# Optimization experiments

Measured on AMD Instinct MI355X. Metric: run time of the kernel, lower is better.

Reference implementation:

```python
import jax, jax.numpy as jnp
import numpy as np


def _conv(x, w, b=None, stride=1, pad=0, dil=1):
    out = jax.lax.conv_general_dilated(
        x, w, (stride, stride), [(pad, pad), (pad, pad)],
        rhs_dilation=(dil, dil),
        dimension_numbers=('NCHW', 'OIHW', 'NCHW'))
    return out if b is None else out + b[None, :, None, None]


def _sobel_base(out_ch, in_ch, k=3):
    # Exactly mirrors SobelConv2d weight construction (4 directional kernels).
    w = np.zeros((out_ch, in_ch, k, k), np.float32)
    m = k // 2
    for idx in range(out_ch):
        if idx % 4 == 0:
            w[idx, :, 0, :] = -1; w[idx, :, 0, m] = -2
            w[idx, :, -1, :] = 1; w[idx, :, -1, m] = 2
        elif idx % 4 == 1:
            w[idx, :, :, 0] = -1; w[idx, :, m, 0] = -2
            w[idx, :, :, -1] = 1; w[idx, :, m, -1] = 2
        elif idx % 4 == 2:
            w[idx, :, 0, 0] = -2
            for i in range(m + 1):
                w[idx, :, m - i, i] = -1
                w[idx, :, k - 1 - i, m + i] = 1
            w[idx, :, -1, -1] = 2
        else:
            w[idx, :, -1, 0] = -2
            for i in range(m + 1):
                w[idx, :, m + i, i] = -1
                w[idx, :, i, m + i] = 1
            w[idx, :, 0, -1] = 2
    return w


def setup_inputs() -> dict:
    key = jax.random.key(0)
    ks = iter(jax.random.split(key, 40))
    def p(shape, s=0.05):
        return jax.random.normal(next(ks), shape, dtype=jnp.float32) * s
    C = 32  # out_ch == sobel_ch
    f32 = jnp.float32
    return dict(
        x=jax.random.normal(next(ks), (8, 1, 256, 256), dtype=f32),
        sobel_base=jnp.asarray(_sobel_base(C, 1)),
        sobel_factor=jnp.ones((C, 1, 1, 1), f32),
        sobel_bias=jnp.zeros((C,), f32),
        f4_w=p((C, C + 1, 3, 3)), f4_b=jnp.zeros((C,), f32),
        ec1_w=p((C, C, 3, 3)), ec1_b=jnp.zeros((C,), f32),
        ec2_w=p((C, C, 3, 3)), ec2_b=jnp.zeros((C,), f32),
        ec3_w=p((C, C, 3, 3)), ec3_b=jnp.zeros((C,), f32),
        gate_w=p((3, 3 * C, 1, 1)), gate_b=jnp.zeros((3,), f32),
        ca1_w=p((C // 16, C, 1, 1)),  # ChannelAttention fc1 (ratio=16), no bias
        ca2_w=p((C, C // 16, 1, 1)),  # fc2, no bias
        sa_w=p((1, 2, 7, 7)),         # SpatialAttention conv, no bias
        p1_w=p((C, C, 1, 1)), p1_b=jnp.zeros((C,), f32),
        f1_w=p((C, C, 3, 3)), f1_b=jnp.zeros((C,), f32),
        p2_w=p((C, 2 * C, 1, 1)), p2_b=jnp.zeros((C,), f32),
        f2_w=p((C, C, 3, 3)), f2_b=jnp.zeros((C,), f32),
        p3_w=p((C, 2 * C, 1, 1)), p3_b=jnp.zeros((C,), f32),
        f3_w=p((C, C, 3, 3)), f3_b=jnp.zeros((C,), f32),
    )


def reference(x, sobel_base, sobel_factor, sobel_bias, f4_w, f4_b,
              ec1_w, ec1_b, ec2_w, ec2_b, ec3_w, ec3_b, gate_w, gate_b,
              ca1_w, ca2_w, sa_w,
              p1_w, p1_b, f1_w, f1_b, p2_w, p2_b, f2_w, f2_b,
              p3_w, p3_b, f3_w, f3_b):
    lrelu = lambda t: jax.nn.leaky_relu(t, 0.01)
    relu = jax.nn.relu
    # Sobel edge extraction (fixed directional kernels scaled by learned factor)
    out0 = _conv(x, sobel_base * sobel_factor, sobel_bias, pad=1)     # [B,32,H,W]
    out1 = jnp.concatenate([x, out0], axis=1)                          # [B,33,H,W]
    out1 = lrelu(_conv(out1, f4_w, f4_b, pad=1))                       # [B,32,H,W]
    # AdaptiveEdgeConnector: multi-dilation convs + softmax gating
    ex = relu(_conv(out1, ec1_w, ec1_b, pad=1))
    ey = relu(_conv(out1, ec2_w, ec2_b, pad=2, dil=2))
    ez = relu(_conv(out1, ec3_w, ec3_b, pad=3, dil=3))
    gates = jax.nn.softmax(_conv(jnp.concatenate([ex, ey, ez], axis=1), gate_w, gate_b), axis=1)
    enh = gates[:, 0:1] * ex + gates[:, 1:2] * ey + gates[:, 2:3] * ez
    # CBAM: channel attention
    avg = jnp.mean(enh, axis=(2, 3), keepdims=True)
    mx = jnp.max(enh, axis=(2, 3), keepdims=True)
    ca = jax.nn.sigmoid(_conv(relu(_conv(avg, ca1_w)), ca2_w)
                        + _conv(relu(_conv(mx, ca1_w)), ca2_w))
    f = ca * enh
    # CBAM: spatial attention
    sa_in = jnp.concatenate([jnp.mean(f, axis=1, keepdims=True),
                             jnp.max(f, axis=1, keepdims=True)], axis=1)
    sa = jax.nn.sigmoid(_conv(sa_in, sa_w, pad=3))
    edge = sa * f
    # Residual merge + cascaded dense conv stages
    out0 = lrelu(out1 + edge)
    t = lrelu(_conv(out0, p1_w, p1_b))
    t = lrelu(_conv(t, f1_w, f1_b, pad=1))
    o1 = jnp.concatenate([out0, t], axis=1)                            # [B,64,H,W]
    t = lrelu(_conv(o1, p2_w, p2_b))
    t = lrelu(_conv(t, f2_w, f2_b, pad=1))
    o2 = jnp.concatenate([out0, t], axis=1)
    t = lrelu(_conv(o2, p3_w, p3_b))
    t = lrelu(_conv(t, f3_w, f3_b, pad=1))
    return jnp.concatenate([out0, t], axis=1)                          # [B,64,H,W]
```

## Files before the change

### kernel.cpp

```cpp
#include <hip/hip_runtime.h>
#include <math.h>

typedef unsigned short u16;
typedef short short8 __attribute__((ext_vector_type(8)));
typedef float f32x4 __attribute__((ext_vector_type(4)));
typedef unsigned short ushort4v __attribute__((ext_vector_type(4)));

#define Hh 256
#define Ww 256
#define Bb 8
#define PW 262
#define PAD 3
#define HPW (Hh * PW)

__device__ __forceinline__ float bf2f(u16 v) {
    unsigned u = ((unsigned)v) << 16;
    union { unsigned u; float f; } c; c.u = u; return c.f;
}
__device__ __forceinline__ u16 f2bf(float f) {
    union { float f; unsigned u; } c; c.f = f;
    unsigned lsb = (c.u >> 16) & 1u;
    c.u += 0x7fffu + lsb;
    return (u16)(c.u >> 16);
}
__device__ __forceinline__ float sigm(float v) { return 1.f / (1.f + expf(-v)); }

template<int ACT, bool F32OUT, bool FUSEP>
__global__ __launch_bounds__(256) void convs_k(
    const u16* __restrict__ in, const u16* __restrict__ apack,
    const float* __restrict__ bias, void* __restrict__ outp,
    const u16* __restrict__ o0buf, const u16* __restrict__ pw,
    const float* __restrict__ pb, u16* __restrict__ pout)
{
    __shared__ u16 rows[3][4352];
    const int tid = threadIdx.x, lane = tid & 63, wv = tid >> 6;
    const int b = blockIdx.x & 7;
    const int rest = blockIdx.x >> 3;
    const int h = rest >> 1, half = rest & 1;
    const int pl = wv * 32 + (lane & 15);
    const int icg = lane >> 4;

    for (int idx = tid; idx < 3 * 536; idx += 256) {
        int rr = idx / 536, q = idx % 536;
        int r = h - 1 + rr;
        short8 v = (short8){0, 0, 0, 0, 0, 0, 0, 0};
        if ((unsigned)r < 256u)
            v = *(const short8*)(in + ((size_t)b * HPW + (size_t)r * PW + PAD + half * 128 - 3) * 32
                                 + (size_t)q * 8);
        *(short8*)(&rows[rr][q * 8]) = v;
    }
    __syncthreads();

    f32x4 acc[2][2];
    #pragma unroll
    for (int mf = 0; mf < 2; ++mf)
        #pragma unroll
        for (int nf = 0; nf < 2; ++nf)
            acc[mf][nf] = (f32x4){0.f, 0.f, 0.f, 0.f};

    #pragma unroll
    for (int tap = 0; tap < 9; ++tap) {
        const int kh = tap / 3 - 1, kw = tap % 3 - 1;
        const int ri = 1 + kh;
        short8 a0 = *(const short8*)(apack + ((size_t)(tap * 2 + 0) * 64 + lane) * 8);
        short8 a1 = *(const short8*)(apack + ((size_t)(tap * 2 + 1) * 64 + lane) * 8);
        #pragma unroll
        for (int nf = 0; nf < 2; ++nf) {
            short8 bf = *(const short8*)(&rows[ri][(pl + nf * 16 + kw + 3) * 32 + icg * 8]);
            acc[0][nf] = __builtin_amdgcn_mfma_f32_16x16x32_bf16(a0, bf, acc[0][nf], 0, 0, 0);
            acc[1][nf] = __builtin_amdgcn_mfma_f32_16x16x32_bf16(a1, bf, acc[1][nf], 0, 0, 0);
        }
    }
    const int nl = half * 128 + pl;
    f32x4 bi[2];
    bi[0] = *(const f32x4*)(bias + icg * 4);
    bi[1] = *(const f32x4*)(bias + 16 + icg * 4);

    if (FUSEP) {
        u16* tile = &rows[0][0];
        __syncthreads();
        #pragma unroll
        for (int mf = 0; mf < 2; ++mf) {
            const int cob = mf * 16 + icg * 4;
            #pragma unroll
            for (int nf = 0; nf < 2; ++nf) {
                ushort4v o;
                #pragma unroll
                for (int i = 0; i < 4; ++i) {
                    float v = acc[mf][nf][i] + bi[mf][i];
                    v = (v > 0.f) ? v : 0.01f * v;
                    o[i] = f2bf(v);
                }
                *(ushort4v*)(tile + (pl + nf * 16) * 32 + cob) = o;
            }
        }
        __syncthreads();
        f32x4 acc2[2][2];
        #pragma unroll
        for (int mf = 0; mf < 2; ++mf)
            #pragma unroll
            for (int nf = 0; nf < 2; ++nf)
                acc2[mf][nf] = (f32x4){0.f, 0.f, 0.f, 0.f};
        #pragma unroll
        for (int s = 0; s < 2; ++s) {
            short8 pa0 = *(const short8*)(pw + (size_t)(s * 2 + 0) * 512 + lane * 8);
            short8 pa1 = *(const short8*)(pw + (size_t)(s * 2 + 1) * 512 + lane * 8);
            #pragma unroll
            for (int nf = 0; nf < 2; ++nf) {
                const int px = pl + nf * 16;
                short8 bf;
                if (s == 0)
                    bf = *(const short8*)(o0buf + ((size_t)b * HPW + (size_t)h * PW + PAD + half * 128 + px) * 32 + icg * 8);
                else
                    bf = *(const short8*)(tile + px * 32 + icg * 8);
                acc2[0][nf] = __builtin_amdgcn_mfma_f32_16x16x32_bf16(pa0, bf, acc2[0][nf], 0, 0, 0);
                acc2[1][nf] = __builtin_amdgcn_mfma_f32_16x16x32_bf16(pa1, bf, acc2[1][nf], 0, 0, 0);
            }
        }
        const size_t orow = ((size_t)b * HPW + (size_t)h * PW + PAD) * 32;
        #pragma unroll
        for (int mf = 0; mf < 2; ++mf) {
            const int cob = mf * 16 + icg * 4;
            f32x4 pbi = *(const f32x4*)(pb + cob);
            #pragma unroll
            for (int nf = 0; nf < 2; ++nf) {
                ushort4v o;
                #pragma unroll
                for (int i = 0; i < 4; ++i) {
                    float v = acc2[mf][nf][i] + pbi[i];
                    v = (v > 0.f) ? v : 0.01f * v;
                    o[i] = f2bf(v);
                }
                *(ushort4v*)(pout + orow + (size_t)(nl + nf * 16) * 32 + cob) = o;
            }
        }
        if (tid < 12) {
            int col3 = tid >> 2, chunk = tid & 3;
            int col = half ? (256 + PAD + col3) : col3;
            u16* pz = pout + ((size_t)b * HPW + (size_t)h * PW + col) * 32 + chunk * 8;
            *(short8*)pz = (short8){0, 0, 0, 0, 0, 0, 0, 0};
        }
    } else if (F32OUT) {
        float* dp = (float*)outp + ((size_t)b * 64 + 32) * 65536 + (size_t)h * 256;
        #pragma unroll
        for (int mf = 0; mf < 2; ++mf) {
            const int cob = mf * 16 + icg * 4;
            #pragma unroll
            for (int nf = 0; nf < 2; ++nf) {
                const int w = nl + nf * 16;
                #pragma unroll
                for (int i = 0; i < 4; ++i) {
                    float v = acc[mf][nf][i] + bi[mf][i];
                    if (ACT == 1) v = fmaxf(v, 0.f);
                    if (ACT == 2) v = (v > 0.f) ? v : 0.01f * v;
                    dp[(size_t)(cob + i) * 65536 + w] = v;
                }
            }
        }
    } else {
        const size_t orow = ((size_t)b * HPW + (size_t)h * PW + PAD) * 32;
        u16* out = (u16*)outp;
        #pragma unroll
        for (int mf = 0; mf < 2; ++mf) {
            const int cob = mf * 16 + icg * 4;
            #pragma unroll
            for (int nf = 0; nf < 2; ++nf) {
                ushort4v o;
                #pragma unroll
                for (int i = 0; i < 4; ++i) {
                    float v = acc[mf][nf][i] + bi[mf][i];
                    if (ACT == 1) v = fmaxf(v, 0.f);
                    if (ACT == 2) v = (v > 0.f) ? v : 0.01f * v;
                    o[i] = f2bf(v);
                }
                *(ushort4v*)(out + orow + (size_t)(nl + nf * 16) * 32 + cob) = o;
            }
        }
    }
}

__global__ __launch_bounds__(256) void ecfuse_k(
    const u16* __restrict__ in, const u16* __restrict__ apack,
    const float* __restrict__ b1, const float* __restrict__ b2,
    const float* __restrict__ b3, const float* __restrict__ gw_,
    const float* __restrict__ gb_, u16* __restrict__ enh)
{
    __shared__ u16 rows[3][4352];
    __shared__ float gw[288];
    __shared__ float gb[3];
    __shared__ float bs[96];
    int tid = threadIdx.x;
    for (int i = tid; i < 288; i += 256) gw[i] = gw_[i];
    if (tid < 3) gb[tid] = gb_[tid];
    if (tid < 32) bs[tid] = b1[tid];
    else if (tid < 64) bs[tid] = b2[tid - 32];
    else if (tid < 96) bs[tid] = b3[tid - 64];

    const int lane = tid & 63, wv = tid >> 6;
    const int b = blockIdx.x & 7;
    const int rest = blockIdx.x >> 3;
    const int h = rest >> 1, half = rest & 1;
    const int pl = wv * 32 + (lane & 15);
    const int icg = lane >> 4;

    f32x4 acc[3][2][2];
    #pragma unroll
    for (int cv = 0; cv < 3; ++cv)
        #pragma unroll
        for (int mf = 0; mf < 2; ++mf)
            #pragma unroll
            for (int nf = 0; nf < 2; ++nf)
                acc[cv][mf][nf] = (f32x4){0.f, 0.f, 0.f, 0.f};

    #pragma unroll
    for (int cv = 0; cv < 3; ++cv) {
        const int dil = cv + 1;
        __syncthreads();
        for (int idx = tid; idx < 3 * 536; idx += 256) {
            int rr = idx / 536, q = idx % 536;
            int r = h + (rr - 1) * dil;
            short8 v = (short8){0, 0, 0, 0, 0, 0, 0, 0};
            if ((unsigned)r < 256u)
                v = *(const short8*)(in + ((size_t)b * HPW + (size_t)r * PW + PAD + half * 128 - 3) * 32
                                     + (size_t)q * 8);
            *(short8*)(&rows[rr][q * 8]) = v;
        }
        __syncthreads();
        const u16* ap = apack + (size_t)(cv * 9 * 2) * 512;
        #pragma unroll
        for (int tap = 0; tap < 9; ++tap) {
            const int kh = tap / 3 - 1, kw = tap % 3 - 1;
            const int ri = 1 + kh;
            short8 a0 = *(const short8*)(ap + (size_t)(tap * 2 + 0) * 512 + lane * 8);
            short8 a1 = *(const short8*)(ap + (size_t)(tap * 2 + 1) * 512 + lane * 8);
            #pragma unroll
            for (int nf = 0; nf < 2; ++nf) {
                short8 bf = *(const short8*)(&rows[ri][(pl + nf * 16 + kw * dil + 3) * 32 + icg * 8]);
                acc[cv][0][nf] = __builtin_amdgcn_mfma_f32_16x16x32_bf16(a0, bf, acc[cv][0][nf], 0, 0, 0);
                acc[cv][1][nf] = __builtin_amdgcn_mfma_f32_16x16x32_bf16(a1, bf, acc[cv][1][nf], 0, 0, 0);
            }
        }
    }
    const int nl = half * 128 + pl;
    const size_t orow = ((size_t)b * HPW + (size_t)h * PW + PAD) * 32;
    #pragma unroll
    for (int nf = 0; nf < 2; ++nf) {
        float e[3][2][4];
        float g0 = 0.f, g1 = 0.f, g2 = 0.f;
        #pragma unroll
        for (int cv = 0; cv < 3; ++cv)
            #pragma unroll
            for (int mf = 0; mf < 2; ++mf) {
                const int cob = mf * 16 + icg * 4;
                #pragma unroll
                for (int i = 0; i < 4; ++i) {
                    float v = fmaxf(acc[cv][mf][nf][i] + bs[cv * 32 + cob + i], 0.f);
                    e[cv][mf][i] = v;
                    const int c = cv * 32 + cob + i;
                    g0 = fmaf(gw[c], v, g0);
                    g1 = fmaf(gw[96 + c], v, g1);
                    g2 = fmaf(gw[192 + c], v, g2);
                }
            }
        g0 += __shfl_xor(g0, 16); g0 += __shfl_xor(g0, 32);
        g1 += __shfl_xor(g1, 16); g1 += __shfl_xor(g1, 32);
        g2 += __shfl_xor(g2, 16); g2 += __shfl_xor(g2, 32);
        g0 += gb[0]; g1 += gb[1]; g2 += gb[2];
        float m = fmaxf(g0, fmaxf(g1, g2));
        float e0 = expf(g0 - m), e1 = expf(g1 - m), e2 = expf(g2 - m);
        float inv = 1.f / (e0 + e1 + e2);
        e0 *= inv; e1 *= inv; e2 *= inv;
        #pragma unroll
        for (int mf = 0; mf < 2; ++mf) {
            const int cob = mf * 16 + icg * 4;
            ushort4v o;
            #pragma unroll
            for (int i = 0; i < 4; ++i)
                o[i] = f2bf(e0 * e[0][mf][i] + e1 * e[1][mf][i] + e2 * e[2][mf][i]);
            *(ushort4v*)(enh + orow + (size_t)(nl + nf * 16) * 32 + cob) = o;
        }
    }
}

__global__ void prepack_k(
    const float* __restrict__ f4w, const float* __restrict__ e1w,
    const float* __restrict__ e2w, const float* __restrict__ e3w,
    const float* __restrict__ f1w, const float* __restrict__ f2w,
    const float* __restrict__ f3w, const float* __restrict__ p1w,
    const float* __restrict__ p2w, const float* __restrict__ p3w,
    u16* __restrict__ apack)
{
    int gid = blockIdx.x * 256 + threadIdx.x;
    if (gid >= 77 * 1024) return;
    const int offs[11] = {0, 18, 27, 36, 45, 54, 63, 72, 73, 75, 77};
    int step = gid >> 10, r = gid & 1023;
    int layer = 0;
    while (step >= offs[layer + 1]) layer++;
    int s = step - offs[layer];
    int mf = r >> 9, l = (r >> 3) & 63, j = r & 7;
    int co = mf * 16 + (l & 15);
    int ICB = (layer == 0 || layer == 8 || layer == 9) ? 2 : 1;
    int tap = s / ICB, icb = s % ICB;
    int icl = icb * 32 + (l >> 4) * 8 + j;
    float v = 0.f;
    if (layer == 0)      { if (icl < 33) v = f4w[(co * 33 + icl) * 9 + tap]; }
    else if (layer == 1) v = e1w[(co * 32 + icl) * 9 + tap];
    else if (layer == 2) v = e2w[(co * 32 + icl) * 9 + tap];
    else if (layer == 3) v = e3w[(co * 32 + icl) * 9 + tap];
    else if (layer == 4) v = f1w[(co * 32 + icl) * 9 + tap];
    else if (layer == 5) v = f2w[(co * 32 + icl) * 9 + tap];
    else if (layer == 6) v = f3w[(co * 32 + icl) * 9 + tap];
    else if (layer == 7) v = p1w[co * 32 + icl];
    else if (layer == 8) v = p2w[co * 64 + icl];
    else                 v = p3w[co * 64 + icl];
    apack[gid] = f2bf(v);
}

__global__ __launch_bounds__(256) void prep5_k(
    const float* __restrict__ f4w, const float* __restrict__ f4b,
    const float* __restrict__ sbase, const float* __restrict__ sfac,
    const float* __restrict__ sbias,
    float* __restrict__ w5, float* __restrict__ be)
{
    __shared__ float sF[32 * 33 * 9];
    __shared__ float sS[288];
    __shared__ float sBias[32];
    int t = threadIdx.x;
    for (int i = t; i < 32 * 33 * 9; i += 256) sF[i] = f4w[i];
    for (int i = t; i < 288; i += 256) sS[i] = sbase[i] * sfac[i / 9];
    if (t < 32) sBias[t] = sbias[t];
    __syncthreads();

    for (int idx = t; idx < 800; idx += 256) {
        int co = idx / 25, tap = idx % 25, kh = tap / 5, kw = tap % 5;
        float s = 0.f;
        if (kh >= 1 && kh <= 3 && kw >= 1 && kw <= 3)
            s = sF[(co * 33 + 0) * 9 + (kh - 1) * 3 + (kw - 1)];
        for (int sc = 0; sc < 32; ++sc) {
            #pragma unroll
            for (int a = 0; a < 3; ++a)
                #pragma unroll
                for (int bq = 0; bq < 3; ++bq) {
                    int p = kh - a, q = kw - bq;
                    if (p >= 0 && p < 3 && q >= 0 && q < 3)
                        s = fmaf(sF[(co * 33 + 1 + sc) * 9 + a * 3 + bq],
                                 sS[sc * 9 + p * 3 + q], s);
                }
        }
        w5[idx] = s;
    }
    for (int co = t; co < 32; co += 256) {
        float s = f4b[co];
        for (int sc = 0; sc < 32; ++sc) {
            float wsum = 0.f;
            #pragma unroll
            for (int k = 0; k < 9; ++k) wsum += sF[(co * 33 + 1 + sc) * 9 + k];
            s = fmaf(sBias[sc], wsum, s);
        }
        be[co] = s;
    }
}

__global__ __launch_bounds__(256) void conv5_k(
    const float* __restrict__ x, const float* __restrict__ w5,
    const float* __restrict__ be, u16* __restrict__ out1)
{
    __shared__ float sw[800];
    __shared__ float sb[32];
    int tid = threadIdx.x;
    for (int i = tid; i < 800; i += 256) sw[i] = w5[i];
    if (tid < 32) sb[tid] = be[tid];
    __syncthreads();
    int b = blockIdx.x & 7, h = blockIdx.x >> 3, w = tid;
    const float* xp = x + (size_t)b * 65536;
    float xv[25];
    #pragma unroll
    for (int i = 0; i < 5; ++i) {
        int r = h + i - 2;
        #pragma unroll
        for (int j = 0; j < 5; ++j) {
            int c = w + j - 2;
            xv[i * 5 + j] = ((unsigned)r < 256u && (unsigned)c < 256u)
                            ? xp[r * 256 + c] : 0.f;
        }
    }
    u16* dst = out1 + ((size_t)b * HPW + (size_t)h * PW + PAD + w) * 32;
    #pragma unroll
    for (int cb = 0; cb < 4; ++cb) {
        short8 o;
        #pragma unroll
        for (int j = 0; j < 8; ++j) {
            int co = cb * 8 + j;
            float s = sb[co];
            #pragma unroll
            for (int t2 = 0; t2 < 25; ++t2) s = fmaf(sw[co * 25 + t2], xv[t2], s);
            s = (s > 0.f) ? s : 0.01f * s;
            o[j] = (short)f2bf(s);
        }
        *(short8*)(dst + cb * 8) = o;
    }
    if (tid < 24) {
        int col6 = tid >> 2, chunk = tid & 3;
        int col = (col6 < 3) ? col6 : (256 + PAD + col6 - 3);
        u16* pz = out1 + ((size_t)b * HPW + (size_t)h * PW + col) * 32 + chunk * 8;
        *(short8*)pz = (short8){0, 0, 0, 0, 0, 0, 0, 0};
    }
}

__global__ __launch_bounds__(256) void ringfix_k(
    const float* __restrict__ x, const float* __restrict__ f4w,
    const float* __restrict__ f4b, const float* __restrict__ sbase,
    const float* __restrict__ sfac, const float* __restrict__ sbias,
    u16* __restrict__ out1)
{
    __shared__ float sW[288];
    __shared__ float sB[32];
    __shared__ float sF[32 * 33 * 9];
    __shared__ float sO[66][2][32];
    int tid = threadIdx.x;
    for (int i = tid; i < 288; i += 256) sW[i] = sbase[i] * sfac[i / 9];
    if (tid < 32) sB[tid] = sbias[tid];
    for (int i = tid; i < 32 * 33 * 9; i += 256) sF[i] = f4w[i];
    __syncthreads();

    int blk = blockIdx.x;
    int b = blk & 7, rest = blk >> 3;
    int e = rest >> 2, seg = rest & 3;
    const float* xp = x + (size_t)b * 65536;

    for (int i = tid; i < 66 * 2 * 32; i += 256) {
        int sc = i & 31, rr2 = i >> 5;
        int d = rr2 & 1, ul = rr2 >> 1;
        int ug = seg * 64 - 1 + ul;
        float v = 0.f;
        if ((unsigned)ug < 256u) {
            int h, w;
            if (e == 0)      { h = d;        w = ug; }
            else if (e == 1) { h = 255 - d;  w = ug; }
            else if (e == 2) { h = ug;       w = d; }
            else             { h = ug;       w = 255 - d; }
            float s = sB[sc];
            for (int p = 0; p < 3; ++p)
                for (int q = 0; q < 3; ++q) {
                    int rr = h + p - 1, cc = w + q - 1;
                    if ((unsigned)rr < 256u && (unsigned)cc < 256u)
                        s = fmaf(sW[sc * 9 + p * 3 + q], xp[rr * 256 + cc], s);
                }
            v = s;
        }
        sO[ul][d][sc] = v;
    }
    __syncthreads();

    int pi = tid & 63, cog = tid >> 6;
    int up = seg * 64 + pi;
    int h, w;
    if (e == 0)      { h = 0;   w = up; }
    else if (e == 1) { h = 255; w = up; }
    else if (e == 2) { h = up;  w = 0; }
    else             { h = up;  w = 255; }
    short8 ov;
    for (int cj = 0; cj < 8; ++cj) {
        int co = cog * 8 + cj;
        float acc = f4b[co];
        for (int a = 0; a < 3; ++a)
            for (int bb = 0; bb < 3; ++bb) {
                int hh = h + a - 1, ww = w + bb - 1;
                if ((unsigned)hh < 256u && (unsigned)ww < 256u)
                    acc = fmaf(sF[(co * 33) * 9 + a * 3 + bb], xp[hh * 256 + ww], acc);
                int d, ug;
                if (e == 0)      { d = hh;        ug = ww; }
                else if (e == 1) { d = 255 - hh;  ug = ww; }
                else if (e == 2) { d = ww;        ug = hh; }
                else             { d = 255 - ww;  ug = hh; }
                if (d >= 0 && d < 2 && (unsigned)ug < 256u) {
                    int ul = ug - (seg * 64 - 1);
                    for (int sc = 0; sc < 32; ++sc)
                        acc = fmaf(sF[(co * 33 + 1 + sc) * 9 + a * 3 + bb], sO[ul][d][sc], acc);
                }
            }
        acc = (acc > 0.f) ? acc : 0.01f * acc;
        ov[cj] = (short)f2bf(acc);
    }
    u16* dst = out1 + ((size_t)b * HPW + (size_t)h * PW + PAD + w) * 32 + cog * 8;
    *(short8*)dst = ov;
}

__global__ __launch_bounds__(256) void ca_part_k(
    const u16* __restrict__ enh, float* __restrict__ part)
{
    int blk = blockIdx.x, b = blk & 7, sl = blk >> 3;
    int tid = threadIdx.x, lane = tid & 63, wv = tid >> 6;
    float s[32], m[32];
    #pragma unroll
    for (int c = 0; c < 32; ++c) { s[c] = 0.f; m[c] = -1e30f; }
    for (int k = 0; k < 8; ++k) {
        int px = sl * 2048 + k * 256 + tid;
        int h = px >> 8, w = px & 255;
        size_t off = ((size_t)b * HPW + (size_t)h * PW + PAD + w) * 32;
        #pragma unroll
        for (int cb = 0; cb < 4; ++cb) {
            short8 v = *(const short8*)(enh + off + cb * 8);
            #pragma unroll
            for (int j = 0; j < 8; ++j) {
                float f = bf2f((u16)v[j]);
                s[cb * 8 + j] += f;
                m[cb * 8 + j] = fmaxf(m[cb * 8 + j], f);
            }
        }
    }
    #pragma unroll
    for (int c = 0; c < 32; ++c)
        #pragma unroll
        for (int o = 32; o; o >>= 1) {
            s[c] += __shfl_down(s[c], o);
            m[c] = fmaxf(m[c], __shfl_down(m[c], o));
        }
    __shared__ float ls[4][32], lm[4][32];
    if (lane == 0)
        for (int c = 0; c < 32; ++c) { ls[wv][c] = s[c]; lm[wv][c] = m[c]; }
    __syncthreads();
    if (tid < 32) {
        float ts = 0.f, tm = -1e30f;
        for (int w2 = 0; w2 < 4; ++w2) { ts += ls[w2][tid]; tm = fmaxf(tm, lm[w2][tid]); }
        int bs = b * 32 + sl;
        part[(size_t)(bs * 2 + 0) * 32 + tid] = ts;
        part[(size_t)(bs * 2 + 1) * 32 + tid] = tm;
    }
}

__global__ void ca_final_k(const float* __restrict__ part,
                           const float* __restrict__ w1, const float* __restrict__ w2,
                           float* __restrict__ ca)
{
    int t = threadIdx.x, b = t >> 5, c = t & 31;
    float s = 0.f, m = -1e30f;
    for (int sl = 0; sl < 32; ++sl) {
        int bs = b * 32 + sl;
        s += part[(size_t)(bs * 2 + 0) * 32 + c];
        m = fmaxf(m, part[(size_t)(bs * 2 + 1) * 32 + c]);
    }
    __shared__ float av[8][32], mx[8][32];
    av[b][c] = s * (1.f / 65536.f);
    mx[b][c] = m;
    __syncthreads();
    float sa0 = 0.f, sm0 = 0.f, sa1 = 0.f, sm1 = 0.f;
    for (int k = 0; k < 32; ++k) {
        float wa = w1[k], wb = w1[32 + k];
        sa0 = fmaf(wa, av[b][k], sa0); sm0 = fmaf(wa, mx[b][k], sm0);
        sa1 = fmaf(wb, av[b][k], sa1); sm1 = fmaf(wb, mx[b][k], sm1);
    }
    float h0 = fmaxf(sa0, 0.f) + fmaxf(sm0, 0.f);
    float h1 = fmaxf(sa1, 0.f) + fmaxf(sm1, 0.f);
    ca[t] = sigm(w2[c * 2 + 0] * h0 + w2[c * 2 + 1] * h1);
}

__global__ __launch_bounds__(256) void samap_k(
    const u16* __restrict__ enh, const float* __restrict__ ca,
    float* __restrict__ smap)
{
    __shared__ float sca[256];
    int tid = threadIdx.x;
    sca[tid] = ca[tid];
    __syncthreads();
    int b = blockIdx.x & 7;
    int r = (blockIdx.x >> 3) * 256 + tid;
    if (r >= 262 * 262) return;
    int ph = r / 262, pw = r % 262;
    float mean = 0.f, mxv = 0.f;
    if (ph >= 3 && ph < 259 && pw >= 3 && pw < 259) {
        int h = ph - 3, w = pw - 3;
        size_t off = ((size_t)b * HPW + (size_t)h * PW + PAD + w) * 32;
        float s = 0.f, m = -1e30f;
        #pragma unroll
        for (int cb = 0; cb < 4; ++cb) {
            short8 v = *(const short8*)(enh + off + cb * 8);
            #pragma unroll
            for (int j = 0; j < 8; ++j) {
                float f = bf2f((u16)v[j]) * sca[b * 32 + cb * 8 + j];
                s += f; m = fmaxf(m, f);
            }
        }
        mean = s * (1.f / 32.f); mxv = m;
    }
    smap[((size_t)b * 262 * 262 + (size_t)ph * 262 + pw) * 2 + 0] = mean;
    smap[((size_t)b * 262 * 262 + (size_t)ph * 262 + pw) * 2 + 1] = mxv;
}

__global__ __launch_bounds__(256) void merge_k(
    const float* __restrict__ smap, const float* __restrict__ saw,
    const float* __restrict__ ca, const u16* __restrict__ out1,
    const u16* __restrict__ enh, u16* __restrict__ o0,
    float* __restrict__ dout,
    const u16* __restrict__ ap1, const float* __restrict__ p1b,
    u16* __restrict__ p1out)
{
    __shared__ float sw[98];
    __shared__ float sca[256];
    __shared__ u16 tile[256 * 32];
    int tid = threadIdx.x;
    for (int i = tid; i < 98; i += 256) sw[i] = saw[i];
    sca[tid] = ca[tid];
    __syncthreads();
    int b = blockIdx.x & 7;
    int h = blockIdx.x >> 3;
    int w = tid;
    const float* sp = smap + (size_t)b * 262 * 262 * 2;
    float acc = 0.f;
    #pragma unroll
    for (int kh = 0; kh < 7; ++kh)
        #pragma unroll
        for (int kw = 0; kw < 7; ++kw) {
            const float* q = sp + ((size_t)(h + kh) * 262 + (w + kw)) * 2;
            acc = fmaf(q[0], sw[kh * 7 + kw], acc);
            acc = fmaf(q[1], sw[49 + kh * 7 + kw], acc);
        }
    float sa = sigm(acc);
    size_t off = ((size_t)b * HPW + (size_t)h * PW + PAD + w) * 32;
    float* dp = dout + (size_t)b * 64 * 65536 + (size_t)h * 256 + w;
    #pragma unroll
    for (int cb = 0; cb < 4; ++cb) {
        short8 ve = *(const short8*)(enh + off + cb * 8);
        short8 vo = *(const short8*)(out1 + off + cb * 8);
        short8 o;
        #pragma unroll
        for (int j = 0; j < 8; ++j) {
            float f = sca[b * 32 + cb * 8 + j] * bf2f((u16)ve[j]);
            float v = bf2f((u16)vo[j]) + sa * f;
            v = (v > 0.f) ? v : 0.01f * v;
            o[j] = (short)f2bf(v);
            dp[(size_t)(cb * 8 + j) * 65536] = v;
        }
        *(short8*)(o0 + off + cb * 8) = o;
        *(short8*)(&tile[w * 32 + cb * 8]) = o;
    }
    __syncthreads();
    const int lane = tid & 63, wv = tid >> 6;
    const int icg = lane >> 4, l15 = lane & 15;
    f32x4 acc1[2][4];
    #pragma unroll
    for (int mf = 0; mf < 2; ++mf)
        #pragma unroll
        for (int nf = 0; nf < 4; ++nf)
            acc1[mf][nf] = (f32x4){0.f, 0.f, 0.f, 0.f};
    short8 pa0 = *(const short8*)(ap1 + (size_t)0 * 512 + lane * 8);
    short8 pa1 = *(const short8*)(ap1 + (size_t)1 * 512 + lane * 8);
    #pragma unroll
    for (int nf = 0; nf < 4; ++nf) {
        short8 bf = *(const short8*)(&tile[(wv * 64 + l15 + nf * 16) * 32 + icg * 8]);
        acc1[0][nf] = __builtin_amdgcn_mfma_f32_16x16x32_bf16(pa0, bf, acc1[0][nf], 0, 0, 0);
        acc1[1][nf] = __builtin_amdgcn_mfma_f32_16x16x32_bf16(pa1, bf, acc1[1][nf], 0, 0, 0);
    }
    const size_t orow = ((size_t)b * HPW + (size_t)h * PW + PAD) * 32;
    #pragma unroll
    for (int mf = 0; mf < 2; ++mf) {
        const int cob = mf * 16 + icg * 4;
        f32x4 pbi = *(const f32x4*)(p1b + cob);
        #pragma unroll
        for (int nf = 0; nf < 4; ++nf) {
            const int px = wv * 64 + l15 + nf * 16;
            ushort4v o;
            #pragma unroll
            for (int i = 0; i < 4; ++i) {
                float v = acc1[mf][nf][i] + pbi[i];
                v = (v > 0.f) ? v : 0.01f * v;
                o[i] = f2bf(v);
            }
            *(ushort4v*)(p1out + orow + (size_t)px * 32 + cob) = o;
        }
    }
}

extern "C" void kernel_launch(void* const* d_in, const int* in_sizes, int n_in,
                              void* d_out, int out_size, void* d_ws, size_t ws_size,
                              hipStream_t stream)
{
    (void)in_sizes; (void)n_in; (void)out_size; (void)ws_size;
    const float* x        = (const float*)d_in[0];
    const float* sob_base = (const float*)d_in[1];
    const float* sob_fac  = (const float*)d_in[2];
    const float* sob_bias = (const float*)d_in[3];
    const float* f4_w = (const float*)d_in[4];   const float* f4_b = (const float*)d_in[5];
    const float* ec1_w = (const float*)d_in[6];  const float* ec1_b = (const float*)d_in[7];
    const float* ec2_w = (const float*)d_in[8];  const float* ec2_b = (const float*)d_in[9];
    const float* ec3_w = (const float*)d_in[10]; const float* ec3_b = (const float*)d_in[11];
    const float* gate_w = (const float*)d_in[12]; const float* gate_b = (const float*)d_in[13];
    const float* ca1_w = (const float*)d_in[14]; const float* ca2_w = (const float*)d_in[15];
    const float* sa_w  = (const float*)d_in[16];
    const float* p1_w = (const float*)d_in[17]; const float* p1_b = (const float*)d_in[18];
    const float* f1_w = (const float*)d_in[19]; const float* f1_b = (const float*)d_in[20];
    const float* p2_w = (const float*)d_in[21]; const float* p2_b = (const float*)d_in[22];
    const float* f2_w = (const float*)d_in[23]; const float* f2_b = (const float*)d_in[24];
    const float* p3_w = (const float*)d_in[25]; const float* p3_b = (const float*)d_in[26];
    const float* f3_w = (const float*)d_in[27]; const float* f3_b = (const float*)d_in[28];

    const size_t PB32 = (size_t)Bb * HPW * 32 * 2;
    char* ws = (char*)d_ws;
    u16* Q    = (u16*)(ws);
    u16* O0   = (u16*)(ws + PB32);
    u16* T    = (u16*)(ws + 2 * PB32);
    u16* ENH  = (u16*)(ws + 3 * PB32);
    u16* AP   = (u16*)(ws + 4 * PB32);
    float* W5   = (float*)(ws + 4 * PB32 + 77 * 1024 * 2);
    float* BE   = W5 + 800;
    float* PART = BE + 32;
    float* CA   = PART + 8 * 32 * 2 * 32;

    char* doutc = (char*)d_out;
    float* SMAP = (float*)(doutc + (134217728 - (size_t)Bb * 262 * 262 * 2 * 4));
    float* dout = (float*)d_out;

    dim3 blk(256);

    prepack_k<<<308, blk, 0, stream>>>(f4_w, ec1_w, ec2_w, ec3_w, f1_w, f2_w, f3_w,
                                       p1_w, p2_w, p3_w, AP);
    prep5_k<<<1, blk, 0, stream>>>(f4_w, f4_b, sob_base, sob_fac, sob_bias, W5, BE);
    conv5_k<<<2048, blk, 0, stream>>>(x, W5, BE, Q);
    ringfix_k<<<128, blk, 0, stream>>>(x, f4_w, f4_b, sob_base, sob_fac, sob_bias, Q);
    ecfuse_k<<<4096, blk, 0, stream>>>(Q, AP + 18 * 1024, ec1_b, ec2_b, ec3_b,
                                       gate_w, gate_b, ENH);
    ca_part_k<<<256, blk, 0, stream>>>(ENH, PART);
    ca_final_k<<<1, blk, 0, stream>>>(PART, ca1_w, ca2_w, CA);
    samap_k<<<2152, blk, 0, stream>>>(ENH, CA, SMAP);
    merge_k<<<2048, blk, 0, stream>>>(SMAP, sa_w, CA, Q, ENH, O0, dout,
                                      AP + 72 * 1024, p1_b, Q);
    convs_k<2, false, true ><<<4096, blk, 0, stream>>>(Q, AP + 45 * 1024, f1_b, nullptr,
                                                       O0, AP + 73 * 1024, p2_b, T);
    convs_k<2, false, true ><<<4096, blk, 0, stream>>>(T, AP + 54 * 1024, f2_b, nullptr,
                                                       O0, AP + 75 * 1024, p3_b, Q);
    convs_k<2, true, false><<<4096, blk, 0, stream>>>(Q, AP + 63 * 1024, f3_b, dout,
                                                      nullptr, nullptr, nullptr, nullptr);
}
```

Baseline: 405.4 us.

## Process two output rows per block in 3x3 conv kernels to reuse halo rows

Each convs_k block now computes two adjacent image rows instead of one. It loads four input rows into shared memory instead of three, and reuses the A-fragment weights across both rows. Grid size halves to match. This cuts redundant halo-row loads and weight fetches per output row. The cost is more accumulator registers, larger shared memory (about 35KB), and fewer blocks, which may lower occupancy.

```diff
diff --git a/kernel.cpp b/kernel.cpp
--- a/kernel.cpp
+++ b/kernel.cpp
@@ -32,17 +32,18 @@
     const u16* __restrict__ o0buf, const u16* __restrict__ pw,
     const float* __restrict__ pb, u16* __restrict__ pout)
 {
-    __shared__ u16 rows[3][4352];
+    __shared__ u16 rows[4][4352];
     const int tid = threadIdx.x, lane = tid & 63, wv = tid >> 6;
     const int b = blockIdx.x & 7;
     const int rest = blockIdx.x >> 3;
-    const int h = rest >> 1, half = rest & 1;
+    const int hpair = rest >> 1, half = rest & 1;
+    const int h0 = hpair * 2;
     const int pl = wv * 32 + (lane & 15);
     const int icg = lane >> 4;
 
-    for (int idx = tid; idx < 3 * 536; idx += 256) {
+    for (int idx = tid; idx < 4 * 536; idx += 256) {
         int rr = idx / 536, q = idx % 536;
-        int r = h - 1 + rr;
+        int r = h0 - 1 + rr;
         short8 v = (short8){0, 0, 0, 0, 0, 0, 0, 0};
         if ((unsigned)r < 256u)
             v = *(const short8*)(in + ((size_t)b * HPW + (size_t)r * PW + PAD + half * 128 - 3) * 32
@@ -51,24 +52,29 @@
     }
     __syncthreads();
 
-    f32x4 acc[2][2];
-    #pragma unroll
-    for (int mf = 0; mf < 2; ++mf)
-        #pragma unroll
-        for (int nf = 0; nf < 2; ++nf)
-            acc[mf][nf] = (f32x4){0.f, 0.f, 0.f, 0.f};
+    f32x4 acc[2][2][2];
+    #pragma unroll
+    for (int r2 = 0; r2 < 2; ++r2)
+        #pragma unroll
+        for (int mf = 0; mf < 2; ++mf)
+            #pragma unroll
+            for (int nf = 0; nf < 2; ++nf)
+                acc[r2][mf][nf] = (f32x4){0.f, 0.f, 0.f, 0.f};
 
     #pragma unroll
     for (int tap = 0; tap < 9; ++tap) {
         const int kh = tap / 3 - 1, kw = tap % 3 - 1;
-        const int ri = 1 + kh;
         short8 a0 = *(const short8*)(apack + ((size_t)(tap * 2 + 0) * 64 + lane) * 8);
         short8 a1 = *(const short8*)(apack + ((size_t)(tap * 2 + 1) * 64 + lane) * 8);
         #pragma unroll
-        for (int nf = 0; nf < 2; ++nf) {
-            short8 bf = *(const short8*)(&rows[ri][(pl + nf * 16 + kw + 3) * 32 + icg * 8]);
-            acc[0][nf] = __builtin_amdgcn_mfma_f32_16x16x32_bf16(a0, bf, acc[0][nf], 0, 0, 0);
-            acc[1][nf] = __builtin_amdgcn_mfma_f32_16x16x32_bf16(a1, bf, acc[1][nf], 0, 0, 0);
+        for (int r2 = 0; r2 < 2; ++r2) {
+            const int ri = 1 + r2 + kh;
+            #pragma unroll
+            for (int nf = 0; nf < 2; ++nf) {
+                short8 bf = *(const short8*)(&rows[ri][(pl + nf * 16 + kw + 3) * 32 + icg * 8]);
+                acc[r2][0][nf] = __builtin_amdgcn_mfma_f32_16x16x32_bf16(a0, bf, acc[r2][0][nf], 0, 0, 0);
+                acc[r2][1][nf] = __builtin_amdgcn_mfma_f32_16x16x32_bf16(a1, bf, acc[r2][1][nf], 0, 0, 0);
+            }
         }
     }
     const int nl = half * 128 + pl;
@@ -80,100 +86,113 @@
         u16* tile = &rows[0][0];
         __syncthreads();
         #pragma unroll
-        for (int mf = 0; mf < 2; ++mf) {
-            const int cob = mf * 16 + icg * 4;
-            #pragma unroll
-            for (int nf = 0; nf < 2; ++nf) {
-                ushort4v o;
+        for (int r2 = 0; r2 < 2; ++r2)
+            #pragma unroll
+            for (int mf = 0; mf < 2; ++mf) {
+                const int cob = mf * 16 + icg * 4;
                 #pragma unroll
-                for (int i = 0; i < 4; ++i) {
-                    float v = acc[mf][nf][i] + bi[mf][i];
-                    v = (v > 0.f) ? v : 0.01f * v;
-                    o[i] = f2bf(v);
-                }
-                *(ushort4v*)(tile + (pl + nf * 16) * 32 + cob) = o;
-            }
-        }
+                for (int nf = 0; nf < 2; ++nf) {
+                    ushort4v o;
+                    #pragma unroll
+                    for (int i = 0; i < 4; ++i) {
+                        float v = acc[r2][mf][nf][i] + bi[mf][i];
+                        v = (v > 0.f) ? v : 0.01f * v;
+                        o[i] = f2bf(v);
+                    }
+                    *(ushort4v*)(tile + ((size_t)(r2 * 128 + pl + nf * 16)) * 32 + cob) = o;
+                }
+            }
         __syncthreads();
-        f32x4 acc2[2][2];
-        #pragma unroll
-        for (int mf = 0; mf < 2; ++mf)
-            #pragma unroll
-            for (int nf = 0; nf < 2; ++nf)
-                acc2[mf][nf] = (f32x4){0.f, 0.f, 0.f, 0.f};
-        #pragma unroll
-        for (int s = 0; s < 2; ++s) {
-            short8 pa0 = *(const short8*)(pw + (size_t)(s * 2 + 0) * 512 + lane * 8);
-            short8 pa1 = *(const short8*)(pw + (size_t)(s * 2 + 1) * 512 + lane * 8);
-            #pragma unroll
-            for (int nf = 0; nf < 2; ++nf) {
-                const int px = pl + nf * 16;
-                short8 bf;
-                if (s == 0)
-                    bf = *(const short8*)(o0buf + ((size_t)b * HPW + (size_t)h * PW + PAD + half * 128 + px) * 32 + icg * 8);
-                else
-                    bf = *(const short8*)(tile + px * 32 + icg * 8);
-                acc2[0][nf] = __builtin_amdgcn_mfma_f32_16x16x32_bf16(pa0, bf, acc2[0][nf], 0, 0, 0);
-                acc2[1][nf] = __builtin_amdgcn_mfma_f32_16x16x32_bf16(pa1, bf, acc2[1][nf], 0, 0, 0);
-            }
-        }
-        const size_t orow = ((size_t)b * HPW + (size_t)h * PW + PAD) * 32;
-        #pragma unroll
-        for (int mf = 0; mf < 2; ++mf) {
-            const int cob = mf * 16 + icg * 4;
-            f32x4 pbi = *(const f32x4*)(pb + cob);
-            #pragma unroll
-            for (int nf = 0; nf < 2; ++nf) {
-                ushort4v o;
+        #pragma unroll
+        for (int r2 = 0; r2 < 2; ++r2) {
+            const int h = h0 + r2;
+            f32x4 acc2[2][2];
+            #pragma unroll
+            for (int mf = 0; mf < 2; ++mf)
                 #pragma unroll
-                for (int i = 0; i < 4; ++i) {
-                    float v = acc2[mf][nf][i] + pbi[i];
-                    v = (v > 0.f) ? v : 0.01f * v;
-                    o[i] = f2bf(v);
-                }
-                *(ushort4v*)(pout + orow + (size_t)(nl + nf * 16) * 32 + cob) = o;
-            }
-        }
-        if (tid < 12) {
-            int col3 = tid >> 2, chunk = tid & 3;
+                for (int nf = 0; nf < 2; ++nf)
+                    acc2[mf][nf] = (f32x4){0.f, 0.f, 0.f, 0.f};
+            #pragma unroll
+            for (int s = 0; s < 2; ++s) {
+                short8 pa0 = *(const short8*)(pw + (size_t)(s * 2 + 0) * 512 + lane * 8);
+                short8 pa1 = *(const short8*)(pw + (size_t)(s * 2 + 1) * 512 + lane * 8);
+                #pragma unroll
+                for (int nf = 0; nf < 2; ++nf) {
+                    const int px = pl + nf * 16;
+                    short8 bf;
+                    if (s == 0)
+                        bf = *(const short8*)(o0buf + ((size_t)b * HPW + (size_t)h * PW + PAD + half * 128 + px) * 32 + icg * 8);
+                    else
+                        bf = *(const short8*)(tile + ((size_t)(r2 * 128 + px)) * 32 + icg * 8);
+                    acc2[0][nf] = __builtin_amdgcn_mfma_f32_16x16x32_bf16(pa0, bf, acc2[0][nf], 0, 0, 0);
+                    acc2[1][nf] = __builtin_amdgcn_mfma_f32_16x16x32_bf16(pa1, bf, acc2[1][nf], 0, 0, 0);
+                }
+            }
+            const size_t orow = ((size_t)b * HPW + (size_t)h * PW + PAD) * 32;
+            #pragma unroll
+            for (int mf = 0; mf < 2; ++mf) {
+                const int cob = mf * 16 + icg * 4;
+                f32x4 pbi = *(const f32x4*)(pb + cob);
+                #pragma unroll
+                for (int nf = 0; nf < 2; ++nf) {
+                    ushort4v o;
+                    #pragma unroll
+                    for (int i = 0; i < 4; ++i) {
+                        float v = acc2[mf][nf][i] + pbi[i];
+                        v = (v > 0.f) ? v : 0.01f * v;
+                        o[i] = f2bf(v);
+                    }
+                    *(ushort4v*)(pout + orow + (size_t)(nl + nf * 16) * 32 + cob) = o;
+                }
+            }
+        }
+        if (tid < 24) {
+            int r2 = tid / 12, rem = tid % 12;
+            int col3 = rem >> 2, chunk = rem & 3;
             int col = half ? (256 + PAD + col3) : col3;
-            u16* pz = pout + ((size_t)b * HPW + (size_t)h * PW + col) * 32 + chunk * 8;
+            u16* pz = pout + ((size_t)b * HPW + (size_t)(h0 + r2) * PW + col) * 32 + chunk * 8;
             *(short8*)pz = (short8){0, 0, 0, 0, 0, 0, 0, 0};
         }
     } else if (F32OUT) {
-        float* dp = (float*)outp + ((size_t)b * 64 + 32) * 65536 + (size_t)h * 256;
-        #pragma unroll
-        for (int mf = 0; mf < 2; ++mf) {
-            const int cob = mf * 16 + icg * 4;
-            #pragma unroll
-            for (int nf = 0; nf < 2; ++nf) {
-                const int w = nl + nf * 16;
+        #pragma unroll
+        for (int r2 = 0; r2 < 2; ++r2) {
+            float* dp = (float*)outp + ((size_t)b * 64 + 32) * 65536 + (size_t)(h0 + r2) * 256;
+            #pragma unroll
+            for (int mf = 0; mf < 2; ++mf) {
+                const int cob = mf * 16 + icg * 4;
                 #pragma unroll
-                for (int i = 0; i < 4; ++i) {
-                    float v = acc[mf][nf][i] + bi[mf][i];
-                    if (ACT == 1) v = fmaxf(v, 0.f);
-                    if (ACT == 2) v = (v > 0.f) ? v : 0.01f * v;
-                    dp[(size_t)(cob + i) * 65536 + w] = v;
+                for (int nf = 0; nf < 2; ++nf) {
+                    const int w = nl + nf * 16;
+                    #pragma unroll
+                    for (int i = 0; i < 4; ++i) {
+                        float v = acc[r2][mf][nf][i] + bi[mf][i];
+                        if (ACT == 1) v = fmaxf(v, 0.f);
+                        if (ACT == 2) v = (v > 0.f) ? v : 0.01f * v;
+                        dp[(size_t)(cob + i) * 65536 + w] = v;
+                    }
                 }
             }
         }
     } else {
-        const size_t orow = ((size_t)b * HPW + (size_t)h * PW + PAD) * 32;
         u16* out = (u16*)outp;
         #pragma unroll
-        for (int mf = 0; mf < 2; ++mf) {
-            const int cob = mf * 16 + icg * 4;
-            #pragma unroll
-            for (int nf = 0; nf < 2; ++nf) {
-                ushort4v o;
+        for (int r2 = 0; r2 < 2; ++r2) {
+            const size_t orow = ((size_t)b * HPW + (size_t)(h0 + r2) * PW + PAD) * 32;
+            #pragma unroll
+            for (int mf = 0; mf < 2; ++mf) {
+                const int cob = mf * 16 + icg * 4;
                 #pragma unroll
-                for (int i = 0; i < 4; ++i) {
-                    float v = acc[mf][nf][i] + bi[mf][i];
-                    if (ACT == 1) v = fmaxf(v, 0.f);
-                    if (ACT == 2) v = (v > 0.f) ? v : 0.01f * v;
-                    o[i] = f2bf(v);
-                }
-                *(ushort4v*)(out + orow + (size_t)(nl + nf * 16) * 32 + cob) = o;
+                for (int nf = 0; nf < 2; ++nf) {
+                    ushort4v o;
+                    #pragma unroll
+                    for (int i = 0; i < 4; ++i) {
+                        float v = acc[r2][mf][nf][i] + bi[mf][i];
+                        if (ACT == 1) v = fmaxf(v, 0.f);
+                        if (ACT == 2) v = (v > 0.f) ? v : 0.01f * v;
+                        o[i] = f2bf(v);
+                    }
+                    *(ushort4v*)(out + orow + (size_t)(nl + nf * 16) * 32 + cob) = o;
+                }
             }
         }
     }
@@ -724,10 +743,10 @@
     samap_k<<<2152, blk, 0, stream>>>(ENH, CA, SMAP);
     merge_k<<<2048, blk, 0, stream>>>(SMAP, sa_w, CA, Q, ENH, O0, dout,
                                       AP + 72 * 1024, p1_b, Q);
-    convs_k<2, false, true ><<<4096, blk, 0, stream>>>(Q, AP + 45 * 1024, f1_b, nullptr,
+    convs_k<2, false, true ><<<2048, blk, 0, stream>>>(Q, AP + 45 * 1024, f1_b, nullptr,
                                                        O0, AP + 73 * 1024, p2_b, T);
-    convs_k<2, false, true ><<<4096, blk, 0, stream>>>(T, AP + 54 * 1024, f2_b, nullptr,
+    convs_k<2, false, true ><<<2048, blk, 0, stream>>>(T, AP + 54 * 1024, f2_b, nullptr,
                                                        O0, AP + 75 * 1024, p3_b, Q);
-    convs_k<2, true, false><<<4096, blk, 0, stream>>>(Q, AP + 63 * 1024, f3_b, dout,
+    convs_k<2, true, false><<<2048, blk, 0, stream>>>(Q, AP + 63 * 1024, f3_b, dout,
                                                       nullptr, nullptr, nullptr, nullptr);
 }
```

Result: no change. 399.2 us (median of 2 runs) (-1.5%).
